# Optimization experiments

Measured on AMD Instinct MI355X. Metric: run time of the kernel, lower is better.

Reference implementation:

```python
import jax, jax.numpy as jnp
import numpy as np

N_NODES = 50000
N_EDGES = 1_600_000
IN_CH = 128
HIDDEN = 64
OUT_CH = 1


def glorot(key, shape):
    limit = np.sqrt(6.0 / (shape[0] + shape[1]))
    return jax.random.uniform(key, shape, jnp.float32, -limit, limit)


def setup_inputs() -> dict:
    key = jax.random.key(0)
    ks = jax.random.split(key, 6)
    x = jax.random.normal(ks[0], (N_NODES, IN_CH), jnp.float32)
    edge_index = jax.random.randint(ks[1], (2, N_EDGES), 0, N_NODES, jnp.int64)
    W1 = glorot(ks[2], (IN_CH, HIDDEN))
    b1 = jnp.zeros((HIDDEN,), jnp.float32)
    W2 = glorot(ks[3], (HIDDEN, HIDDEN // 2))
    b2 = jnp.zeros((HIDDEN // 2,), jnp.float32)
    Wh = glorot(ks[4], (HIDDEN // 2, OUT_CH))
    bh = jnp.zeros((OUT_CH,), jnp.float32)
    return {"x": x, "edge_index": edge_index, "W1": W1, "b1": b1,
            "W2": W2, "b2": b2, "Wh": Wh, "bh": bh}


def gcn_conv(x, src, dst, W, b):
    """PyG-style GCNConv: H' = D^{-1/2} (A + I) D^{-1/2} X W + b."""
    n = x.shape[0]
    h = x @ W  # transform first (smaller message dim)
    # degree of A + I (all edge weights = 1, self-loop weight = 1)
    deg = jax.ops.segment_sum(jnp.ones(src.shape[0], h.dtype), dst,
                              num_segments=n) + 1.0
    dinv = deg ** -0.5
    norm = dinv[src] * dinv[dst]                      # [E]
    msg = h[src] * norm[:, None]                      # [E, F] gather
    agg = jax.ops.segment_sum(msg, dst, num_segments=n)  # scatter-add
    agg = agg + h * (dinv * dinv)[:, None]            # self-loop term
    return agg + b


def reference(x, edge_index, W1, b1, W2, b2, Wh, bh):
    src, dst = edge_index[0], edge_index[1]
    h = jax.nn.relu(gcn_conv(x, src, dst, W1, b1))
    # dropout: inference mode (training=False) -> identity
    h = jax.nn.relu(gcn_conv(h, src, dst, W2, b2))
    return h @ Wh + bh
```

## Files before the change

### kernel.cpp

```cpp
#include <hip/hip_runtime.h>

#define N_NODES 50000
#define IN_CH 128
#define HID 64
#define HID2 32

constexpr int NB = 391;
constexpr int CHUNK = 4096;
constexpr int CAP = 5120;
#define FPSCALE 524288.0f
#define FPINV   0x1p-19f
#define T1SCALE 2048.0f
#define T1INV   0x1p-11f

typedef short short2e __attribute__((ext_vector_type(2)));

__device__ __forceinline__ unsigned short f2bf(float f) {
    union { float f; unsigned u; } v; v.f = f;
    unsigned r = v.u + 0x7fff + ((v.u >> 16) & 1);
    return (unsigned short)(r >> 16);
}
__device__ __forceinline__ float bflo(unsigned d) {
    union { unsigned u; float f; } v; v.u = d << 16; return v.f;
}
__device__ __forceinline__ float bfhi(unsigned d) {
    union { unsigned u; float f; } v; v.u = d & 0xffff0000u; return v.f;
}
__device__ __forceinline__ unsigned pack16(int a, int b) {
    return ((unsigned)a & 0xffffu) | ((unsigned)b << 16);
}
__device__ __forceinline__ unsigned pkadd(unsigned a, unsigned b) {
    short2e x, y, r;
    __builtin_memcpy(&x, &a, 4);
    __builtin_memcpy(&y, &b, 4);
    r = x + y;
    unsigned d;
    __builtin_memcpy(&d, &r, 4);
    return d;
}
__device__ __forceinline__ int lo16(unsigned u) { return (int)(short)(u & 0xffffu); }
__device__ __forceinline__ int hi16(unsigned u) { return ((int)u) >> 16; }
__device__ __forceinline__ void acc2(int& a0, int& a1, unsigned u) {
    a0 += (int)(short)(u & 0xffffu);
    a1 += ((int)u) >> 16;
}

__global__ __launch_bounds__(1024) void bin_kernel(const int* __restrict__ src,
                                                   const int* __restrict__ dst,
                                                   int* __restrict__ bcur,
                                                   unsigned short* __restrict__ psrc,
                                                   unsigned char* __restrict__ pbyte, int E) {
    __shared__ int hist[NB], lbase[NB], gbase[NB], lcur[NB];
    __shared__ unsigned outp[CHUNK];
    __shared__ int wsum[16];
    int tid = threadIdx.x, lane = tid & 63;
    int base = blockIdx.x * CHUNK;
    int cnt = min(CHUNK, E - base);
    for (int i = tid; i < NB; i += 1024) hist[i] = 0;
    int es[CHUNK / 1024], ed[CHUNK / 1024];
    __syncthreads();
#pragma unroll
    for (int k = 0; k < CHUNK / 1024; k++) {
        int e = base + k * 1024 + tid;
        if (e < E) {
            es[k] = src[e];
            ed[k] = dst[e];
            atomicAdd(&hist[ed[k] >> 7], 1);
        }
    }
    __syncthreads();
    {
        int v = (tid < NB) ? hist[tid] : 0;
        int s = v;
#pragma unroll
        for (int d = 1; d < 64; d <<= 1) {
            int t = __shfl_up(s, d, 64);
            if (lane >= d) s += t;
        }
        if (lane == 63 && tid < 512) wsum[tid >> 6] = s;
        __syncthreads();
        if (tid == 0) {
            int run = 0;
#pragma unroll
            for (int w = 0; w < 8; w++) { int t = wsum[w]; wsum[w] = run; run += t; }
        }
        __syncthreads();
        if (tid < NB) lbase[tid] = wsum[tid >> 6] + s - v;
    }
    __syncthreads();
    for (int i = tid; i < NB; i += 1024) {
        gbase[i] = i * CAP + (hist[i] ? atomicAdd(&bcur[i], hist[i]) : 0);
        lcur[i] = lbase[i];
    }
    __syncthreads();
#pragma unroll
    for (int k = 0; k < CHUNK / 1024; k++) {
        int e = base + k * 1024 + tid;
        if (e < E) {
            int b = ed[k] >> 7;
            int p = atomicAdd(&lcur[b], 1);
            outp[p] = ((unsigned)es[k] << 16) | (unsigned)ed[k];
        }
    }
    __syncthreads();
#pragma unroll
    for (int k = 0; k < CHUNK / 1024; k++) {
        int i = k * 1024 + tid;
        if (i < cnt) {
            unsigned p = outp[i];
            int d = (int)(p & 0xffffu);
            int b = d >> 7;
            int gp = gbase[b] + (i - lbase[b]);
            psrc[gp] = (unsigned short)(p >> 16);
            pbyte[gp] = (unsigned char)(d & 127);
        }
    }
}

__global__ __launch_bounds__(1024) void fine_kernel(unsigned short* __restrict__ psrc,
                                                    const unsigned char* __restrict__ pbyte,
                                                    const int* __restrict__ bcur,
                                                    uint2* __restrict__ meta,
                                                    float* __restrict__ dinv, int N) {
    __shared__ unsigned short lsrc[CAP];
    __shared__ unsigned char lb[CAP];
    __shared__ int fh[128], fb[128], fc[128];
    __shared__ int wsum2[2];
    int b = blockIdx.x, tid = threadIdx.x, lane = tid & 63;
    int gb = b * CAP;
    int cnt = min(bcur[b], CAP);
    if (tid < 128) fh[tid] = 0;
    __syncthreads();
    for (int i = tid; i < cnt; i += 1024) {
        lsrc[i] = psrc[gb + i];
        int dl = pbyte[gb + i];
        lb[i] = (unsigned char)dl;
        atomicAdd(&fh[dl], 1);
    }
    __syncthreads();
    {
        int v = (tid < 128) ? fh[tid] : 0;
        int s = v;
#pragma unroll
        for (int d = 1; d < 64; d <<= 1) {
            int t = __shfl_up(s, d, 64);
            if (lane >= d) s += t;
        }
        if (lane == 63 && tid < 128) wsum2[tid >> 6] = s;
        __syncthreads();
        if (tid < 128) fb[tid] = ((tid >> 6) ? wsum2[0] : 0) + s - v;
    }
    __syncthreads();
    if (tid < 128) {
        fc[tid] = fb[tid];
        int node = (b << 7) + tid;
        if (node < N) {
            meta[node] = make_uint2((unsigned)(gb + fb[tid]), (unsigned)fh[tid]);
            dinv[node] = rsqrtf((float)fh[tid] + 1.0f);
        }
    }
    __syncthreads();
    for (int i = tid; i < cnt; i += 1024) {
        int p = atomicAdd(&fc[lb[i]], 1);
        psrc[gb + p] = lsrc[i];
    }
}

template <int K, int J, int NPB>
__global__ __launch_bounds__(256) void gemm_s_kernel(const float* __restrict__ X,
                                                     const float* __restrict__ W,
                                                     const float* __restrict__ dinv,
                                                     short* __restrict__ out, int N) {
    constexpr int QJ = J / 4;
    constexpr int NPT = NPB / (256 / QJ);
    static_assert(NPT == 2, "layout assumes 2 nodes/thread");
    constexpr int RG = K / 4;
    constexpr int RS = K + 4;
    __shared__ float Ws[K * J];
    __shared__ float Xs[NPB * RS];
    int tid = threadIdx.x;
    if (blockIdx.x == 0 && tid < J / 2)
        ((unsigned*)(out + (size_t)N * J))[tid] = 0;
    for (int i = tid; i < K * J / 4; i += 256) ((float4*)Ws)[i] = ((const float4*)W)[i];
    int n0 = blockIdx.x * NPB;
    for (int i = tid; i < NPB * RG; i += 256) {
        int r = i / RG, c = i % RG;
        int n = n0 + r;
        float4 v = make_float4(0.f, 0.f, 0.f, 0.f);
        if (n < N) v = ((const float4*)(X + (size_t)n * K))[c];
        *(float4*)&Xs[r * RS + ((c ^ (r & 7)) << 2)] = v;
    }
    __syncthreads();
    int q = tid % QJ, g = (tid / QJ) * NPT;
    const float* xr0 = &Xs[g * RS];
    const float* xr1 = &Xs[(g + 1) * RS];
    int sw0 = g & 7, sw1 = (g + 1) & 7;
    float4 a0 = make_float4(0.f, 0.f, 0.f, 0.f);
    float4 a1 = make_float4(0.f, 0.f, 0.f, 0.f);
#pragma unroll 8
    for (int k = 0; k < K; k++) {
        float4 w = *(const float4*)&Ws[k * J + q * 4];
        float x0 = xr0[(((k >> 2) ^ sw0) << 2) + (k & 3)];
        float x1 = xr1[(((k >> 2) ^ sw1) << 2) + (k & 3)];
        a0.x += x0 * w.x; a0.y += x0 * w.y; a0.z += x0 * w.z; a0.w += x0 * w.w;
        a1.x += x1 * w.x; a1.y += x1 * w.y; a1.z += x1 * w.z; a1.w += x1 * w.w;
    }
#pragma unroll
    for (int t = 0; t < NPT; t++) {
        int n = n0 + g + t;
        if (n < N) {
            float4 a = t ? a1 : a0;
            float d0 = dinv[n] * T1SCALE;
            int v0 = max(-16383, min(16383, (int)lrintf(a.x * d0)));
            int v1 = max(-16383, min(16383, (int)lrintf(a.y * d0)));
            int v2 = max(-16383, min(16383, (int)lrintf(a.z * d0)));
            int v3 = max(-16383, min(16383, (int)lrintf(a.w * d0)));
            *(uint2*)(out + (size_t)n * J + q * 4) = make_uint2(pack16(v0, v1), pack16(v2, v3));
        }
    }
}

__global__ __launch_bounds__(256) void agg1_fused_kernel(const unsigned short* __restrict__ sorted_src,
                                                         const uint2* __restrict__ meta,
                                                         const short* __restrict__ xtab,
                                                         const float* __restrict__ b1,
                                                         const float* __restrict__ W2,
                                                         unsigned short* __restrict__ hws, int N) {
    __shared__ float hrow[4][HID];
    int tid = threadIdx.x, wid = tid >> 6, lane = tid & 63;
    if (blockIdx.x == 0 && tid < HID2 / 2)
        ((unsigned*)(hws + (size_t)N * HID2))[tid] = 0;
    int n = blockIdx.x * 4 + wid;
    if (n >= N) return;
    int g = lane >> 3, fl = lane & 7;
    uint2 mm = meta[n];
    int start = (int)mm.x, len_ = (int)mm.y;
    float dvn = rsqrtf((float)len_ + 1.0f);
    const unsigned* tb = (const unsigned*)xtab;
    const unsigned char* tbb = (const unsigned char*)xtab;
    int acc[8] = {0, 0, 0, 0, 0, 0, 0, 0};
    if (len_ <= 64) {
        int sall = (lane < len_) ? (int)sorted_src[start + lane] : N;
        unsigned fo = ((unsigned)fl) << 4;
        int s0 = __shfl(sall, g, 64);
        int s1 = __shfl(sall, g + 8, 64);
        int s2 = __shfl(sall, g + 16, 64);
        int s3 = __shfl(sall, g + 24, 64);
        if (len_ <= 32) {
            uint4 q0 = *(const uint4*)(tbb + ((((unsigned)s0) << 7) + fo));
            uint4 q1 = *(const uint4*)(tbb + ((((unsigned)s1) << 7) + fo));
            uint4 q2 = *(const uint4*)(tbb + ((((unsigned)s2) << 7) + fo));
            uint4 q3 = *(const uint4*)(tbb + ((((unsigned)s3) << 7) + fo));
            unsigned pa0 = pkadd(q0.x, q1.x), pa1 = pkadd(q0.y, q1.y);
            unsigned pa2 = pkadd(q0.z, q1.z), pa3 = pkadd(q0.w, q1.w);
            unsigned pb0 = pkadd(q2.x, q3.x), pb1 = pkadd(q2.y, q3.y);
            unsigned pb2 = pkadd(q2.z, q3.z), pb3 = pkadd(q2.w, q3.w);
            acc[0] = lo16(pa0) + lo16(pb0); acc[1] = hi16(pa0) + hi16(pb0);
            acc[2] = lo16(pa1) + lo16(pb1); acc[3] = hi16(pa1) + hi16(pb1);
            acc[4] = lo16(pa2) + lo16(pb2); acc[5] = hi16(pa2) + hi16(pb2);
            acc[6] = lo16(pa3) + lo16(pb3); acc[7] = hi16(pa3) + hi16(pb3);
        } else {
            int s4 = __shfl(sall, g + 32, 64);
            int s5 = __shfl(sall, g + 40, 64);
            int s6 = __shfl(sall, g + 48, 64);
            int s7 = __shfl(sall, g + 56, 64);
            uint4 q0 = *(const uint4*)(tbb + ((((unsigned)s0) << 7) + fo));
            uint4 q1 = *(const uint4*)(tbb + ((((unsigned)s1) << 7) + fo));
            uint4 q2 = *(const uint4*)(tbb + ((((unsigned)s2) << 7) + fo));
            uint4 q3 = *(const uint4*)(tbb + ((((unsigned)s3) << 7) + fo));
            uint4 q4 = *(const uint4*)(tbb + ((((unsigned)s4) << 7) + fo));
            uint4 q5 = *(const uint4*)(tbb + ((((unsigned)s5) << 7) + fo));
            uint4 q6 = *(const uint4*)(tbb + ((((unsigned)s6) << 7) + fo));
            uint4 q7 = *(const uint4*)(tbb + ((((unsigned)s7) << 7) + fo));
            unsigned pa0 = pkadd(q0.x, q1.x), pa1 = pkadd(q0.y, q1.y);
            unsigned pa2 = pkadd(q0.z, q1.z), pa3 = pkadd(q0.w, q1.w);
            unsigned pb0 = pkadd(q2.x, q3.x), pb1 = pkadd(q2.y, q3.y);
            unsigned pb2 = pkadd(q2.z, q3.z), pb3 = pkadd(q2.w, q3.w);
            unsigned pc0 = pkadd(q4.x, q5.x), pc1 = pkadd(q4.y, q5.y);
            unsigned pc2 = pkadd(q4.z, q5.z), pc3 = pkadd(q4.w, q5.w);
            unsigned pd0 = pkadd(q6.x, q7.x), pd1 = pkadd(q6.y, q7.y);
            unsigned pd2 = pkadd(q6.z, q7.z), pd3 = pkadd(q6.w, q7.w);
            acc[0] = (lo16(pa0) + lo16(pb0)) + (lo16(pc0) + lo16(pd0));
            acc[1] = (hi16(pa0) + hi16(pb0)) + (hi16(pc0) + hi16(pd0));
            acc[2] = (lo16(pa1) + lo16(pb1)) + (lo16(pc1) + lo16(pd1));
            acc[3] = (hi16(pa1) + hi16(pb1)) + (hi16(pc1) + hi16(pd1));
            acc[4] = (lo16(pa2) + lo16(pb2)) + (lo16(pc2) + lo16(pd2));
            acc[5] = (hi16(pa2) + hi16(pb2)) + (hi16(pc2) + hi16(pd2));
            acc[6] = (lo16(pa3) + lo16(pb3)) + (lo16(pc3) + lo16(pd3));
            acc[7] = (hi16(pa3) + hi16(pb3)) + (hi16(pc3) + hi16(pd3));
        }
    } else {
        int i = start + g, end = start + len_;
        for (; i < end; i += 8) {
            int s = sorted_src[i];
            uint4 q = *(const uint4*)(tb + (size_t)s * 32 + fl * 4);
            acc2(acc[0], acc[1], q.x); acc2(acc[2], acc[3], q.y);
            acc2(acc[4], acc[5], q.z); acc2(acc[6], acc[7], q.w);
        }
    }
#pragma unroll
    for (int m = 8; m <= 32; m <<= 1)
#pragma unroll
        for (int j = 0; j < 8; j++) acc[j] += __shfl_xor(acc[j], m, 64);
    if (g == 0) {
        float dis = dvn * T1INV;
        uint4 q = *(const uint4*)(tb + (size_t)n * 32 + fl * 4);
        int sv[8];
        sv[0] = (int)(short)(q.x & 0xffffu); sv[1] = ((int)q.x) >> 16;
        sv[2] = (int)(short)(q.y & 0xffffu); sv[3] = ((int)q.y) >> 16;
        sv[4] = (int)(short)(q.z & 0xffffu); sv[5] = ((int)q.z) >> 16;
        sv[6] = (int)(short)(q.w & 0xffffu); sv[7] = ((int)q.w) >> 16;
        float4 bb0 = *(const float4*)(b1 + fl * 8);
        float4 bb1 = *(const float4*)(b1 + fl * 8 + 4);
        float bbv[8] = {bb0.x, bb0.y, bb0.z, bb0.w, bb1.x, bb1.y, bb1.z, bb1.w};
        float o[8];
#pragma unroll
        for (int j = 0; j < 8; j++)
            o[j] = fmaxf((float)(acc[j] + sv[j]) * dis + bbv[j], 0.f);
        *(float4*)&hrow[wid][fl * 8]     = make_float4(o[0], o[1], o[2], o[3]);
        *(float4*)&hrow[wid][fl * 8 + 4] = make_float4(o[4], o[5], o[6], o[7]);
    }
    int j = lane & 31, half = lane >> 5;
    const float* hb = &hrow[wid][half << 5];
    const float* w2b = W2 + ((half << 5) * HID2) + j;
    float p = 0.f;
#pragma unroll
    for (int k4 = 0; k4 < 8; k4++) {
        float4 h4 = *(const float4*)(hb + (k4 << 2));
        p += h4.x * w2b[(k4 * 4 + 0) * HID2];
        p += h4.y * w2b[(k4 * 4 + 1) * HID2];
        p += h4.z * w2b[(k4 * 4 + 2) * HID2];
        p += h4.w * w2b[(k4 * 4 + 3) * HID2];
    }
    p += __shfl_xor(p, 32, 64);
    if (lane < 32)
        hws[(size_t)n * HID2 + j] = f2bf(p * dvn * FPSCALE);
}

__global__ __launch_bounds__(256) void agg2_final_kernel(const unsigned short* __restrict__ sorted_src,
                                                         const uint2* __restrict__ meta,
                                                         const unsigned short* __restrict__ hws,
                                                         const float* __restrict__ b2,
                                                         const float* __restrict__ Wh,
                                                         const float* __restrict__ bh,
                                                         float* __restrict__ out, int N) {
    int lane = threadIdx.x & 63;
    int n = blockIdx.x * 4 + (threadIdx.x >> 6);
    if (n >= N) return;
    int g = lane >> 2, fl = lane & 3;
    uint2 mm = meta[n];
    int start = (int)mm.x, len_ = (int)mm.y;
    float dvn = rsqrtf((float)len_ + 1.0f);
    const unsigned char* hbb = (const unsigned char*)hws;
    float af[8] = {0.f, 0.f, 0.f, 0.f, 0.f, 0.f, 0.f, 0.f};
    unsigned fo = ((unsigned)fl) << 4;
    if (len_ <= 64) {
        int sall = (lane < len_) ? (int)sorted_src[start + lane] : N;
        int s0 = __shfl(sall, g, 64);
        int s1 = __shfl(sall, g + 16, 64);
        int s2 = __shfl(sall, g + 32, 64);
        int s3 = __shfl(sall, g + 48, 64);
        uint4 q0 = *(const uint4*)(hbb + ((((unsigned)s0) << 6) + fo));
        uint4 q1 = *(const uint4*)(hbb + ((((unsigned)s1) << 6) + fo));
        uint4 q2 = *(const uint4*)(hbb + ((((unsigned)s2) << 6) + fo));
        uint4 q3 = *(const uint4*)(hbb + ((((unsigned)s3) << 6) + fo));
        af[0] = (bflo(q0.x) + bflo(q1.x)) + (bflo(q2.x) + bflo(q3.x));
        af[1] = (bfhi(q0.x) + bfhi(q1.x)) + (bfhi(q2.x) + bfhi(q3.x));
        af[2] = (bflo(q0.y) + bflo(q1.y)) + (bflo(q2.y) + bflo(q3.y));
        af[3] = (bfhi(q0.y) + bfhi(q1.y)) + (bfhi(q2.y) + bfhi(q3.y));
        af[4] = (bflo(q0.z) + bflo(q1.z)) + (bflo(q2.z) + bflo(q3.z));
        af[5] = (bfhi(q0.z) + bfhi(q1.z)) + (bfhi(q2.z) + bfhi(q3.z));
        af[6] = (bflo(q0.w) + bflo(q1.w)) + (bflo(q2.w) + bflo(q3.w));
        af[7] = (bfhi(q0.w) + bfhi(q1.w)) + (bfhi(q2.w) + bfhi(q3.w));
    } else {
        int i = start + g, end = start + len_;
        for (; i < end; i += 16) {
            int s = sorted_src[i];
            uint4 q = *(const uint4*)(hbb + ((((unsigned)s) << 6) + fo));
            af[0] += bflo(q.x); af[1] += bfhi(q.x);
            af[2] += bflo(q.y); af[3] += bfhi(q.y);
            af[4] += bflo(q.z); af[5] += bfhi(q.z);
            af[6] += bflo(q.w); af[7] += bfhi(q.w);
        }
    }
#pragma unroll
    for (int m = 4; m <= 32; m <<= 1)
#pragma unroll
        for (int j = 0; j < 8; j++) af[j] += __shfl_xor(af[j], m, 64);
    float dis = dvn * FPINV;
    uint4 q = *(const uint4*)(hbb + ((((unsigned)n) << 6) + fo));
    float sf[8] = {bflo(q.x), bfhi(q.x), bflo(q.y), bfhi(q.y),
                   bflo(q.z), bfhi(q.z), bflo(q.w), bfhi(q.w)};
    float4 bb0 = *(const float4*)(b2 + fl * 8);
    float4 bb1 = *(const float4*)(b2 + fl * 8 + 4);
    float bbv[8] = {bb0.x, bb0.y, bb0.z, bb0.w, bb1.x, bb1.y, bb1.z, bb1.w};
    float4 wv0 = *(const float4*)(Wh + fl * 8);
    float4 wv1 = *(const float4*)(Wh + fl * 8 + 4);
    float wvv[8] = {wv0.x, wv0.y, wv0.z, wv0.w, wv1.x, wv1.y, wv1.z, wv1.w};
    float p = 0.f;
#pragma unroll
    for (int j = 0; j < 8; j++)
        p += fmaxf((af[j] + sf[j]) * dis + bbv[j], 0.f) * wvv[j];
    p += __shfl_xor(p, 1, 64);
    p += __shfl_xor(p, 2, 64);
    if (lane == 0) out[n] = p + bh[0];
}

extern "C" void kernel_launch(void* const* d_in, const int* in_sizes, int n_in,
                              void* d_out, int out_size, void* d_ws, size_t ws_size,
                              hipStream_t stream) {
    const float* x  = (const float*)d_in[0];
    const int*   ei = (const int*)d_in[1];
    const float* W1 = (const float*)d_in[2];
    const float* b1 = (const float*)d_in[3];
    const float* W2 = (const float*)d_in[4];
    const float* b2 = (const float*)d_in[5];
    const float* Wh = (const float*)d_in[6];
    const float* bh = (const float*)d_in[7];
    float* out = (float*)d_out;

    const int N = N_NODES;
    const int E = in_sizes[1] / 2;
    const int* src = ei;
    const int* dst = ei + E;

    int* ws = (int*)d_ws;
    int*            bcur  = ws;
    uint2*          meta  = (uint2*)(bcur + 512);
    float*          dinv  = (float*)(meta + 50048);
    unsigned short* psrc  = (unsigned short*)(dinv + 50048);
    unsigned char*  pbyte = (unsigned char*)(psrc + (size_t)NB * CAP);
    short*          xtab  = (short*)(pbyte + (size_t)NB * CAP);
    unsigned short* hws   = (unsigned short*)(xtab + (size_t)(N + 1) * HID);

    hipMemsetAsync(bcur, 0, NB * sizeof(int), stream);

    int eblocks = (E + CHUNK - 1) / CHUNK;
    bin_kernel<<<eblocks, 1024, 0, stream>>>(src, dst, bcur, psrc, pbyte, E);
    fine_kernel<<<NB, 1024, 0, stream>>>(psrc, pbyte, bcur, meta, dinv, N);

    gemm_s_kernel<IN_CH, HID, 32><<<(N + 31) / 32, 256, 0, stream>>>(x, W1, dinv, xtab, N);
    agg1_fused_kernel<<<(N + 3) / 4, 256, 0, stream>>>(psrc, meta, xtab, b1, W2, hws, N);
    agg2_final_kernel<<<(N + 3) / 4, 256, 0, stream>>>(psrc, meta, hws, b2, Wh, bh, out, N);
}
```

Baseline: 188.9 us.

## Split layer-1 aggregation into two 32-feature passes over half-width tables

The 64-wide int16 transformed-feature table is split into two 32-column tables (xlo, xhi), and layer-1 aggregation runs as two kernels, each gathering 64-byte rows. This shrinks the gather working set per pass so it fits better in cache. The first pass writes its half of the hidden row to an fp32 scratch buffer that the second pass reloads before the W2 projection. In exchange it adds a kernel launch, a second read of the edge lists, and an extra scratch write/read, and it also switches some loads and stores to nontemporal hints.

```diff
diff --git a/kernel.cpp b/kernel.cpp
--- a/kernel.cpp
+++ b/kernel.cpp
@@ -14,6 +14,7 @@
 #define T1INV   0x1p-11f
 
 typedef short short2e __attribute__((ext_vector_type(2)));
+typedef float floatx4 __attribute__((ext_vector_type(4)));
 
 __device__ __forceinline__ unsigned short f2bf(float f) {
     union { float f; unsigned u; } v; v.f = f;
@@ -170,7 +171,8 @@
 __global__ __launch_bounds__(256) void gemm_s_kernel(const float* __restrict__ X,
                                                      const float* __restrict__ W,
                                                      const float* __restrict__ dinv,
-                                                     short* __restrict__ out, int N) {
+                                                     short* __restrict__ xlo,
+                                                     short* __restrict__ xhi, int N) {
     constexpr int QJ = J / 4;
     constexpr int NPT = NPB / (256 / QJ);
     static_assert(NPT == 2, "layout assumes 2 nodes/thread");
@@ -179,8 +181,10 @@
     __shared__ float Ws[K * J];
     __shared__ float Xs[NPB * RS];
     int tid = threadIdx.x;
-    if (blockIdx.x == 0 && tid < J / 2)
-        ((unsigned*)(out + (size_t)N * J))[tid] = 0;
+    if (blockIdx.x == 0) {
+        if (tid < 16) ((unsigned*)(xlo + (size_t)N * 32))[tid] = 0;
+        else if (tid < 32) ((unsigned*)(xhi + (size_t)N * 32))[tid - 16] = 0;
+    }
     for (int i = tid; i < K * J / 4; i += 256) ((float4*)Ws)[i] = ((const float4*)W)[i];
     int n0 = blockIdx.x * NPB;
     for (int i = tid; i < NPB * RG; i += 256) {
@@ -215,42 +219,48 @@
             int v1 = max(-16383, min(16383, (int)lrintf(a.y * d0)));
             int v2 = max(-16383, min(16383, (int)lrintf(a.z * d0)));
             int v3 = max(-16383, min(16383, (int)lrintf(a.w * d0)));
-            *(uint2*)(out + (size_t)n * J + q * 4) = make_uint2(pack16(v0, v1), pack16(v2, v3));
-        }
-    }
-}
-
-__global__ __launch_bounds__(256) void agg1_fused_kernel(const unsigned short* __restrict__ sorted_src,
-                                                         const uint2* __restrict__ meta,
-                                                         const short* __restrict__ xtab,
-                                                         const float* __restrict__ b1,
-                                                         const float* __restrict__ W2,
-                                                         unsigned short* __restrict__ hws, int N) {
-    __shared__ float hrow[4][HID];
-    int tid = threadIdx.x, wid = tid >> 6, lane = tid & 63;
-    if (blockIdx.x == 0 && tid < HID2 / 2)
-        ((unsigned*)(hws + (size_t)N * HID2))[tid] = 0;
-    int n = blockIdx.x * 4 + wid;
+            short* op = (q < 8) ? (xlo + (size_t)n * 32 + q * 4)
+                                : (xhi + (size_t)n * 32 + (q - 8) * 4);
+            *(uint2*)op = make_uint2(pack16(v0, v1), pack16(v2, v3));
+        }
+    }
+}
+
+__global__ __launch_bounds__(256) void agg1a_kernel(const unsigned short* __restrict__ sorted_src,
+                                                    const uint2* __restrict__ meta,
+                                                    const short* __restrict__ xlo,
+                                                    const float* __restrict__ b1,
+                                                    float* __restrict__ hlo, int N) {
+    int tid = threadIdx.x, lane = tid & 63;
+    int n = blockIdx.x * 4 + (tid >> 6);
     if (n >= N) return;
-    int g = lane >> 3, fl = lane & 7;
+    int g = lane >> 2, fl = lane & 3;
     uint2 mm = meta[n];
     int start = (int)mm.x, len_ = (int)mm.y;
     float dvn = rsqrtf((float)len_ + 1.0f);
-    const unsigned* tb = (const unsigned*)xtab;
-    const unsigned char* tbb = (const unsigned char*)xtab;
+    const unsigned char* tbb = (const unsigned char*)xlo;
     int acc[8] = {0, 0, 0, 0, 0, 0, 0, 0};
+    unsigned fo = ((unsigned)fl) << 4;
     if (len_ <= 64) {
-        int sall = (lane < len_) ? (int)sorted_src[start + lane] : N;
-        unsigned fo = ((unsigned)fl) << 4;
+        int sall = (lane < len_) ? (int)__builtin_nontemporal_load(sorted_src + start + lane) : N;
         int s0 = __shfl(sall, g, 64);
-        int s1 = __shfl(sall, g + 8, 64);
-        int s2 = __shfl(sall, g + 16, 64);
-        int s3 = __shfl(sall, g + 24, 64);
+        int s1 = __shfl(sall, g + 16, 64);
         if (len_ <= 32) {
-            uint4 q0 = *(const uint4*)(tbb + ((((unsigned)s0) << 7) + fo));
-            uint4 q1 = *(const uint4*)(tbb + ((((unsigned)s1) << 7) + fo));
-            uint4 q2 = *(const uint4*)(tbb + ((((unsigned)s2) << 7) + fo));
-            uint4 q3 = *(const uint4*)(tbb + ((((unsigned)s3) << 7) + fo));
+            uint4 q0 = *(const uint4*)(tbb + ((((unsigned)s0) << 6) + fo));
+            uint4 q1 = *(const uint4*)(tbb + ((((unsigned)s1) << 6) + fo));
+            unsigned p0 = pkadd(q0.x, q1.x), p1 = pkadd(q0.y, q1.y);
+            unsigned p2 = pkadd(q0.z, q1.z), p3 = pkadd(q0.w, q1.w);
+            acc[0] = lo16(p0); acc[1] = hi16(p0);
+            acc[2] = lo16(p1); acc[3] = hi16(p1);
+            acc[4] = lo16(p2); acc[5] = hi16(p2);
+            acc[6] = lo16(p3); acc[7] = hi16(p3);
+        } else {
+            int s2 = __shfl(sall, g + 32, 64);
+            int s3 = __shfl(sall, g + 48, 64);
+            uint4 q0 = *(const uint4*)(tbb + ((((unsigned)s0) << 6) + fo));
+            uint4 q1 = *(const uint4*)(tbb + ((((unsigned)s1) << 6) + fo));
+            uint4 q2 = *(const uint4*)(tbb + ((((unsigned)s2) << 6) + fo));
+            uint4 q3 = *(const uint4*)(tbb + ((((unsigned)s3) << 6) + fo));
             unsigned pa0 = pkadd(q0.x, q1.x), pa1 = pkadd(q0.y, q1.y);
             unsigned pa2 = pkadd(q0.z, q1.z), pa3 = pkadd(q0.w, q1.w);
             unsigned pb0 = pkadd(q2.x, q3.x), pb1 = pkadd(q2.y, q3.y);
@@ -259,66 +269,122 @@
             acc[2] = lo16(pa1) + lo16(pb1); acc[3] = hi16(pa1) + hi16(pb1);
             acc[4] = lo16(pa2) + lo16(pb2); acc[5] = hi16(pa2) + hi16(pb2);
             acc[6] = lo16(pa3) + lo16(pb3); acc[7] = hi16(pa3) + hi16(pb3);
+        }
+    } else {
+        int i = start + g, end = start + len_;
+        for (; i < end; i += 16) {
+            int s = sorted_src[i];
+            uint4 q = *(const uint4*)(tbb + ((((unsigned)s) << 6) + fo));
+            acc2(acc[0], acc[1], q.x); acc2(acc[2], acc[3], q.y);
+            acc2(acc[4], acc[5], q.z); acc2(acc[6], acc[7], q.w);
+        }
+    }
+#pragma unroll
+    for (int m = 4; m <= 32; m <<= 1)
+#pragma unroll
+        for (int j = 0; j < 8; j++) acc[j] += __shfl_xor(acc[j], m, 64);
+    if (g == 0) {
+        float dis = dvn * T1INV;
+        uint4 q = *(const uint4*)(tbb + ((((unsigned)n) << 6) + fo));
+        int sv[8];
+        sv[0] = lo16(q.x); sv[1] = hi16(q.x); sv[2] = lo16(q.y); sv[3] = hi16(q.y);
+        sv[4] = lo16(q.z); sv[5] = hi16(q.z); sv[6] = lo16(q.w); sv[7] = hi16(q.w);
+        float4 bb0 = *(const float4*)(b1 + fl * 8);
+        float4 bb1 = *(const float4*)(b1 + fl * 8 + 4);
+        float bbv[8] = {bb0.x, bb0.y, bb0.z, bb0.w, bb1.x, bb1.y, bb1.z, bb1.w};
+        float o[8];
+#pragma unroll
+        for (int j = 0; j < 8; j++)
+            o[j] = fmaxf((float)(acc[j] + sv[j]) * dis + bbv[j], 0.f);
+        floatx4* dst0 = (floatx4*)(hlo + (size_t)n * 32 + fl * 8);
+        floatx4 v0 = {o[0], o[1], o[2], o[3]};
+        floatx4 v1 = {o[4], o[5], o[6], o[7]};
+        __builtin_nontemporal_store(v0, dst0);
+        __builtin_nontemporal_store(v1, dst0 + 1);
+    }
+}
+
+__global__ __launch_bounds__(256) void agg1b_kernel(const unsigned short* __restrict__ sorted_src,
+                                                    const uint2* __restrict__ meta,
+                                                    const short* __restrict__ xhi,
+                                                    const float* __restrict__ b1,
+                                                    const float* __restrict__ hlo,
+                                                    const float* __restrict__ W2,
+                                                    unsigned short* __restrict__ hws, int N) {
+    __shared__ float hrow[4][HID];
+    int tid = threadIdx.x, wid = tid >> 6, lane = tid & 63;
+    if (blockIdx.x == 0 && tid < HID2 / 2)
+        ((unsigned*)(hws + (size_t)N * HID2))[tid] = 0;
+    int n = blockIdx.x * 4 + wid;
+    if (n >= N) return;
+    int g = lane >> 2, fl = lane & 3;
+    uint2 mm = meta[n];
+    int start = (int)mm.x, len_ = (int)mm.y;
+    float dvn = rsqrtf((float)len_ + 1.0f);
+    const unsigned char* tbb = (const unsigned char*)xhi;
+    int acc[8] = {0, 0, 0, 0, 0, 0, 0, 0};
+    unsigned fo = ((unsigned)fl) << 4;
+    if (len_ <= 64) {
+        int sall = (lane < len_) ? (int)__builtin_nontemporal_load(sorted_src + start + lane) : N;
+        int s0 = __shfl(sall, g, 64);
+        int s1 = __shfl(sall, g + 16, 64);
+        if (len_ <= 32) {
+            uint4 q0 = *(const uint4*)(tbb + ((((unsigned)s0) << 6) + fo));
+            uint4 q1 = *(const uint4*)(tbb + ((((unsigned)s1) << 6) + fo));
+            unsigned p0 = pkadd(q0.x, q1.x), p1 = pkadd(q0.y, q1.y);
+            unsigned p2 = pkadd(q0.z, q1.z), p3 = pkadd(q0.w, q1.w);
+            acc[0] = lo16(p0); acc[1] = hi16(p0);
+            acc[2] = lo16(p1); acc[3] = hi16(p1);
+            acc[4] = lo16(p2); acc[5] = hi16(p2);
+            acc[6] = lo16(p3); acc[7] = hi16(p3);
         } else {
-            int s4 = __shfl(sall, g + 32, 64);
-            int s5 = __shfl(sall, g + 40, 64);
-            int s6 = __shfl(sall, g + 48, 64);
-            int s7 = __shfl(sall, g + 56, 64);
-            uint4 q0 = *(const uint4*)(tbb + ((((unsigned)s0) << 7) + fo));
-            uint4 q1 = *(const uint4*)(tbb + ((((unsigned)s1) << 7) + fo));
-            uint4 q2 = *(const uint4*)(tbb + ((((unsigned)s2) << 7) + fo));
-            uint4 q3 = *(const uint4*)(tbb + ((((unsigned)s3) << 7) + fo));
-            uint4 q4 = *(const uint4*)(tbb + ((((unsigned)s4) << 7) + fo));
-            uint4 q5 = *(const uint4*)(tbb + ((((unsigned)s5) << 7) + fo));
-            uint4 q6 = *(const uint4*)(tbb + ((((unsigned)s6) << 7) + fo));
-            uint4 q7 = *(const uint4*)(tbb + ((((unsigned)s7) << 7) + fo));
+            int s2 = __shfl(sall, g + 32, 64);
+            int s3 = __shfl(sall, g + 48, 64);
+            uint4 q0 = *(const uint4*)(tbb + ((((unsigned)s0) << 6) + fo));
+            uint4 q1 = *(const uint4*)(tbb + ((((unsigned)s1) << 6) + fo));
+            uint4 q2 = *(const uint4*)(tbb + ((((unsigned)s2) << 6) + fo));
+            uint4 q3 = *(const uint4*)(tbb + ((((unsigned)s3) << 6) + fo));
             unsigned pa0 = pkadd(q0.x, q1.x), pa1 = pkadd(q0.y, q1.y);
             unsigned pa2 = pkadd(q0.z, q1.z), pa3 = pkadd(q0.w, q1.w);
             unsigned pb0 = pkadd(q2.x, q3.x), pb1 = pkadd(q2.y, q3.y);
             unsigned pb2 = pkadd(q2.z, q3.z), pb3 = pkadd(q2.w, q3.w);
-            unsigned pc0 = pkadd(q4.x, q5.x), pc1 = pkadd(q4.y, q5.y);
-            unsigned pc2 = pkadd(q4.z, q5.z), pc3 = pkadd(q4.w, q5.w);
-            unsigned pd0 = pkadd(q6.x, q7.x), pd1 = pkadd(q6.y, q7.y);
-            unsigned pd2 = pkadd(q6.z, q7.z), pd3 = pkadd(q6.w, q7.w);
-            acc[0] = (lo16(pa0) + lo16(pb0)) + (lo16(pc0) + lo16(pd0));
-            acc[1] = (hi16(pa0) + hi16(pb0)) + (hi16(pc0) + hi16(pd0));
-            acc[2] = (lo16(pa1) + lo16(pb1)) + (lo16(pc1) + lo16(pd1));
-            acc[3] = (hi16(pa1) + hi16(pb1)) + (hi16(pc1) + hi16(pd1));
-            acc[4] = (lo16(pa2) + lo16(pb2)) + (lo16(pc2) + lo16(pd2));
-            acc[5] = (hi16(pa2) + hi16(pb2)) + (hi16(pc2) + hi16(pd2));
-            acc[6] = (lo16(pa3) + lo16(pb3)) + (lo16(pc3) + lo16(pd3));
-            acc[7] = (hi16(pa3) + hi16(pb3)) + (hi16(pc3) + hi16(pd3));
+            acc[0] = lo16(pa0) + lo16(pb0); acc[1] = hi16(pa0) + hi16(pb0);
+            acc[2] = lo16(pa1) + lo16(pb1); acc[3] = hi16(pa1) + hi16(pb1);
+            acc[4] = lo16(pa2) + lo16(pb2); acc[5] = hi16(pa2) + hi16(pb2);
+            acc[6] = lo16(pa3) + lo16(pb3); acc[7] = hi16(pa3) + hi16(pb3);
         }
     } else {
         int i = start + g, end = start + len_;
-        for (; i < end; i += 8) {
+        for (; i < end; i += 16) {
             int s = sorted_src[i];
-            uint4 q = *(const uint4*)(tb + (size_t)s * 32 + fl * 4);
+            uint4 q = *(const uint4*)(tbb + ((((unsigned)s) << 6) + fo));
             acc2(acc[0], acc[1], q.x); acc2(acc[2], acc[3], q.y);
             acc2(acc[4], acc[5], q.z); acc2(acc[6], acc[7], q.w);
         }
     }
 #pragma unroll
-    for (int m = 8; m <= 32; m <<= 1)
+    for (int m = 4; m <= 32; m <<= 1)
 #pragma unroll
         for (int j = 0; j < 8; j++) acc[j] += __shfl_xor(acc[j], m, 64);
     if (g == 0) {
         float dis = dvn * T1INV;
-        uint4 q = *(const uint4*)(tb + (size_t)n * 32 + fl * 4);
+        uint4 q = *(const uint4*)(tbb + ((((unsigned)n) << 6) + fo));
         int sv[8];
-        sv[0] = (int)(short)(q.x & 0xffffu); sv[1] = ((int)q.x) >> 16;
-        sv[2] = (int)(short)(q.y & 0xffffu); sv[3] = ((int)q.y) >> 16;
-        sv[4] = (int)(short)(q.z & 0xffffu); sv[5] = ((int)q.z) >> 16;
-        sv[6] = (int)(short)(q.w & 0xffffu); sv[7] = ((int)q.w) >> 16;
-        float4 bb0 = *(const float4*)(b1 + fl * 8);
-        float4 bb1 = *(const float4*)(b1 + fl * 8 + 4);
+        sv[0] = lo16(q.x); sv[1] = hi16(q.x); sv[2] = lo16(q.y); sv[3] = hi16(q.y);
+        sv[4] = lo16(q.z); sv[5] = hi16(q.z); sv[6] = lo16(q.w); sv[7] = hi16(q.w);
+        float4 bb0 = *(const float4*)(b1 + 32 + fl * 8);
+        float4 bb1 = *(const float4*)(b1 + 32 + fl * 8 + 4);
         float bbv[8] = {bb0.x, bb0.y, bb0.z, bb0.w, bb1.x, bb1.y, bb1.z, bb1.w};
         float o[8];
 #pragma unroll
         for (int j = 0; j < 8; j++)
             o[j] = fmaxf((float)(acc[j] + sv[j]) * dis + bbv[j], 0.f);
-        *(float4*)&hrow[wid][fl * 8]     = make_float4(o[0], o[1], o[2], o[3]);
-        *(float4*)&hrow[wid][fl * 8 + 4] = make_float4(o[4], o[5], o[6], o[7]);
+        *(float4*)&hrow[wid][32 + fl * 8]     = make_float4(o[0], o[1], o[2], o[3]);
+        *(float4*)&hrow[wid][32 + fl * 8 + 4] = make_float4(o[4], o[5], o[6], o[7]);
+    }
+    if (lane < 8) {
+        float4 v = *(const float4*)(hlo + (size_t)n * 32 + lane * 4);
+        *(float4*)&hrow[wid][lane * 4] = v;
     }
     int j = lane & 31, half = lane >> 5;
     const float* hb = &hrow[wid][half << 5];
@@ -334,7 +400,7 @@
     }
     p += __shfl_xor(p, 32, 64);
     if (lane < 32)
-        hws[(size_t)n * HID2 + j] = f2bf(p * dvn * FPSCALE);
+        __builtin_nontemporal_store(f2bf(p * dvn * FPSCALE), hws + (size_t)n * HID2 + j);
 }
 
 __global__ __launch_bounds__(256) void agg2_final_kernel(const unsigned short* __restrict__ sorted_src,
@@ -355,7 +421,7 @@
     float af[8] = {0.f, 0.f, 0.f, 0.f, 0.f, 0.f, 0.f, 0.f};
     unsigned fo = ((unsigned)fl) << 4;
     if (len_ <= 64) {
-        int sall = (lane < len_) ? (int)sorted_src[start + lane] : N;
+        int sall = (lane < len_) ? (int)__builtin_nontemporal_load(sorted_src + start + lane) : N;
         int s0 = __shfl(sall, g, 64);
         int s1 = __shfl(sall, g + 16, 64);
         int s2 = __shfl(sall, g + 32, 64);
@@ -430,8 +496,10 @@
     float*          dinv  = (float*)(meta + 50048);
     unsigned short* psrc  = (unsigned short*)(dinv + 50048);
     unsigned char*  pbyte = (unsigned char*)(psrc + (size_t)NB * CAP);
-    short*          xtab  = (short*)(pbyte + (size_t)NB * CAP);
-    unsigned short* hws   = (unsigned short*)(xtab + (size_t)(N + 1) * HID);
+    short*          xlo   = (short*)(pbyte + (size_t)NB * CAP);
+    short*          xhi   = xlo + (size_t)(N + 1) * 32;
+    float*          hlo   = (float*)(xhi + (size_t)(N + 1) * 32);
+    unsigned short* hws   = (unsigned short*)(hlo + (size_t)N * 32);
 
     hipMemsetAsync(bcur, 0, NB * sizeof(int), stream);
 
@@ -439,7 +507,8 @@
     bin_kernel<<<eblocks, 1024, 0, stream>>>(src, dst, bcur, psrc, pbyte, E);
     fine_kernel<<<NB, 1024, 0, stream>>>(psrc, pbyte, bcur, meta, dinv, N);
 
-    gemm_s_kernel<IN_CH, HID, 32><<<(N + 31) / 32, 256, 0, stream>>>(x, W1, dinv, xtab, N);
-    agg1_fused_kernel<<<(N + 3) / 4, 256, 0, stream>>>(psrc, meta, xtab, b1, W2, hws, N);
+    gemm_s_kernel<IN_CH, HID, 32><<<(N + 31) / 32, 256, 0, stream>>>(x, W1, dinv, xlo, xhi, N);
+    agg1a_kernel<<<(N + 3) / 4, 256, 0, stream>>>(psrc, meta, xlo, b1, hlo, N);
+    agg1b_kernel<<<(N + 3) / 4, 256, 0, stream>>>(psrc, meta, xhi, b1, hlo, W2, hws, N);
     agg2_final_kernel<<<(N + 3) / 4, 256, 0, stream>>>(psrc, meta, hws, b2, Wh, bh, out, N);
 }
```

Measured after the change: 215.7 us. 1.14x slower.
